# Kernel tuning notes

Hardware: AMD Instinct MI355X
Metric: run time of the kernel (lower is better)

The kernel has to match this reference:

```python
import jax, jax.numpy as jnp
import numpy as np

BS, L, H, HD, R, HID = 4, 2048, 12, 64, 16, 768


def setup_inputs() -> dict:
    key = jax.random.key(0)
    k0, k1, k2, k3 = jax.random.split(key, 4)
    xavier = np.sqrt(2.0 / (H + HD))  # xavier_normal_ on (H, HD)
    lin = 1.0 / np.sqrt(HID)
    return {
        "hidden_states": jax.random.normal(k0, (BS, L, HID), jnp.float32),
        "K1_w": jax.random.normal(k1, (HID, H * HD), jnp.float32) * lin,
        "K1_b": jnp.zeros((H * HD,), jnp.float32),
        "V1_w": jax.random.normal(k2, (HID, H * HD), jnp.float32) * lin,
        "V1_b": jnp.zeros((H * HD,), jnp.float32),
        "ReadingHead": jax.random.normal(k3, (H, HD), jnp.float32) * xavier,
        "bidirection_weight": jnp.full((1, 1, H, 1, 2 * R), 1.0 / (2 * R), jnp.float32),
    }


def _scan_mmap(valid_mask, reverse):
    # valid_mask: (bs, L, H) bool. Sequential register-shift scan over positions 1..L-1.
    bs, Ln, Hn = valid_mask.shape
    idxs = jnp.arange(1, Ln, dtype=jnp.int32)
    masks = jnp.swapaxes(valid_mask[:, 1:], 0, 1)  # (L-1, bs, H)
    if reverse:
        idxs = idxs[::-1]
        masks = masks[::-1]
    init = jnp.zeros((bs, R + 1, Hn), jnp.int32)

    def step(valids, xm):
        i, m = xm
        valids = valids.at[:, 0].set(i)  # slot 0 <- current index (matches in-place torch order)
        shifted = jnp.where(m[:, None, :], valids[:, :-1], valids[:, 1:])
        valids = valids.at[:, 1:].set(shifted)
        return valids, valids[:, 1:]

    _, out = jax.lax.scan(step, init, (idxs, masks))  # (L-1, bs, R, H)
    if reverse:
        out = out[::-1]
    out = jnp.concatenate([jnp.zeros((1, bs, R, Hn), jnp.int32), out], axis=0)
    return jnp.swapaxes(out, 0, 1)  # (bs, L, R, H)


def reference(hidden_states, K1_w, K1_b, V1_w, V1_b, ReadingHead, bidirection_weight):
    K1 = jax.nn.relu(hidden_states @ K1_w + K1_b).reshape(BS, L, H, HD)
    V1 = jax.nn.relu(hidden_states @ V1_w + V1_b).reshape(BS, L, H, HD)
    dot_products = jnp.einsum('blhn,hn->blh', K1, ReadingHead)
    valid_mask = dot_products > 0.5  # attn_var default branch
    fm = _scan_mmap(valid_mask, False).reshape(BS, L * R, H)
    bm = _scan_mmap(valid_mask, True).reshape(BS, L * R, H)
    V_forward = jnp.take_along_axis(V1, fm[..., None], axis=1).reshape(BS, L, R, H, HD)
    V_backward = jnp.take_along_axis(V1, bm[..., None], axis=1).reshape(BS, L, R, H, HD)
    w = bidirection_weight[0, 0, :, 0, :]  # (H, 2R); first R -> forward, last R -> backward
    ctx = (jnp.einsum('blrhd,hr->blhd', V_forward, w[:, :R])
           + jnp.einsum('blrhd,hr->blhd', V_backward, w[:, R:]))
    return ctx.reshape(BS, L, H * HD)
```

## Files before the change

### kernel.cpp

```cpp
#include <hip/hip_runtime.h>
#include <hip/hip_bf16.h>

#define BS 4
#define L 2048
#define H 12
#define HD 64
#define R 16
#define HID 768
#define MARGIN 0.02f
#define FIXCAP 16384
#define FIXGRID 1024

typedef __attribute__((ext_vector_type(8))) short s8v;
typedef __attribute__((ext_vector_type(4))) float f32x4;

static __device__ __forceinline__ unsigned short f2bf_bits(float f) {
    __hip_bfloat16 h = __float2bfloat16(f);
    return *reinterpret_cast<unsigned short*>(&h);
}

__global__ __launch_bounds__(256) void prep_kernel(
    const float* __restrict__ K1w, const float* __restrict__ V1w,
    __hip_bfloat16* __restrict__ WtK, __hip_bfloat16* __restrict__ WtV,
    int* __restrict__ fixcnt)
{
    if (blockIdx.x == 0 && threadIdx.x == 0) *fixcnt = 0;
    const int t = blockIdx.x;
    const int z = t / 576, rem = t % 576;
    const float* in = z ? V1w : K1w;
    __hip_bfloat16* out = z ? WtV : WtK;
    __shared__ float s[32][33];
    const int c = threadIdx.x & 31, r8 = threadIdx.x >> 5;
    const int kt = (rem / 24) * 32, nt = (rem % 24) * 32;
#pragma unroll
    for (int rr = 0; rr < 4; ++rr) {
        int k = r8 + rr * 8;
        s[k][c] = in[(size_t)(kt + k) * HID + nt + c];
    }
    __syncthreads();
#pragma unroll
    for (int rr = 0; rr < 4; ++rr) {
        int n = r8 + rr * 8;
        out[(size_t)(nt + n) * HID + kt + c] = __float2bfloat16(s[c][n]);
    }
}

__global__ __launch_bounds__(256) void gemm_fused(
    const float* __restrict__ A,
    const __hip_bfloat16* __restrict__ WtK,
    const __hip_bfloat16* __restrict__ WtV,
    const float* __restrict__ K1b,
    const float* __restrict__ V1b,
    const float* __restrict__ RH,
    float* __restrict__ dots,
    int* __restrict__ fixlist,
    int* __restrict__ fixcnt,
    __hip_bfloat16* __restrict__ C)
{
    __shared__ alignas(16) __hip_bfloat16 As[128 * 32];
    __shared__ alignas(16) __hip_bfloat16 Bs[128 * 32];

    const int tid = threadIdx.x;
    const bool isV = blockIdx.y < 6;
    const int m0 = blockIdx.x * 128;
    const int n0 = (isV ? blockIdx.y : blockIdx.y - 6) * 128;
    const __hip_bfloat16* Bt = isV ? WtV : WtK;

    const int wid = tid >> 6, lane = tid & 63;
    const int quad = lane >> 4, lm = lane & 15;
    const int wm = wid & 1, wn = wid >> 1;

    const int r0 = tid >> 2,        c0 = tid & 3;
    const int r1 = (tid + 256) >> 2, c1 = tid & 3;
    const int p0 = c0 ^ ((r0 >> 1) & 3);
    const int p1 = c1 ^ ((r1 >> 1) & 3);

    const float* gA0 = A + (size_t)(m0 + r0) * HID + c0 * 8;
    const float* gA1 = A + (size_t)(m0 + r1) * HID + c1 * 8;
    const __hip_bfloat16* gB0 = Bt + (size_t)(n0 + r0) * HID + c0 * 8;
    const __hip_bfloat16* gB1 = Bt + (size_t)(n0 + r1) * HID + c1 * 8;
    uint4* wA0 = (uint4*)&As[r0 * 32 + p0 * 8];
    uint4* wA1 = (uint4*)&As[r1 * 32 + p1 * 8];
    uint4* wB0 = (uint4*)&Bs[r0 * 32 + p0 * 8];
    uint4* wB1 = (uint4*)&Bs[r1 * 32 + p1 * 8];

    const int fsw = (lm >> 1) & 3;
    const __hip_bfloat16* pA = &As[(wm * 64 + lm) * 32 + ((quad ^ fsw) * 8)];
    const __hip_bfloat16* pB = &Bs[(wn * 64 + lm) * 32 + ((quad ^ fsw) * 8)];

    f32x4 acc[4][4] = {};

    float4 a00 = *(const float4*)gA0, a01 = *(const float4*)(gA0 + 4);
    float4 a10 = *(const float4*)gA1, a11 = *(const float4*)(gA1 + 4);
    uint4  b0  = *(const uint4*)gB0,  b1  = *(const uint4*)gB1;
    gA0 += 32; gA1 += 32; gB0 += 32; gB1 += 32;

    for (int it = 0; it < HID / 32; ++it) {
        union { unsigned short s[8]; uint4 v; } u0, u1;
        u0.s[0] = f2bf_bits(a00.x); u0.s[1] = f2bf_bits(a00.y);
        u0.s[2] = f2bf_bits(a00.z); u0.s[3] = f2bf_bits(a00.w);
        u0.s[4] = f2bf_bits(a01.x); u0.s[5] = f2bf_bits(a01.y);
        u0.s[6] = f2bf_bits(a01.z); u0.s[7] = f2bf_bits(a01.w);
        u1.s[0] = f2bf_bits(a10.x); u1.s[1] = f2bf_bits(a10.y);
        u1.s[2] = f2bf_bits(a10.z); u1.s[3] = f2bf_bits(a10.w);
        u1.s[4] = f2bf_bits(a11.x); u1.s[5] = f2bf_bits(a11.y);
        u1.s[6] = f2bf_bits(a11.z); u1.s[7] = f2bf_bits(a11.w);
        *wA0 = u0.v; *wA1 = u1.v;
        *wB0 = b0;   *wB1 = b1;
        __syncthreads();

        if (it + 1 < HID / 32) {
            a00 = *(const float4*)gA0; a01 = *(const float4*)(gA0 + 4);
            a10 = *(const float4*)gA1; a11 = *(const float4*)(gA1 + 4);
            b0  = *(const uint4*)gB0;  b1  = *(const uint4*)gB1;
            gA0 += 32; gA1 += 32; gB0 += 32; gB1 += 32;
        }

        s8v af[4], bf[4];
#pragma unroll
        for (int i = 0; i < 4; ++i) af[i] = *(const s8v*)(pA + i * 16 * 32);
#pragma unroll
        for (int j = 0; j < 4; ++j) bf[j] = *(const s8v*)(pB + j * 16 * 32);
#pragma unroll
        for (int i = 0; i < 4; ++i)
#pragma unroll
            for (int j = 0; j < 4; ++j)
                acc[i][j] = __builtin_amdgcn_mfma_f32_16x16x32_bf16(
                    af[i], bf[j], acc[i][j], 0, 0, 0);
        __syncthreads();
    }

    if (isV) {
#pragma unroll
        for (int i = 0; i < 4; ++i) {
            int row_b = m0 + wm * 64 + i * 16 + quad * 4;
#pragma unroll
            for (int j = 0; j < 4; ++j) {
                int col = n0 + wn * 64 + j * 16 + lm;
                float bsv = V1b[col];
#pragma unroll
                for (int reg = 0; reg < 4; ++reg) {
                    float v = acc[i][j][reg] + bsv;
                    C[(size_t)(row_b + reg) * HID + col] =
                        __float2bfloat16(fmaxf(v, 0.f));
                }
            }
        }
    } else {
        const int head = (n0 >> 6) + wn;
        float bj[4], rj[4];
#pragma unroll
        for (int j = 0; j < 4; ++j) {
            bj[j] = K1b[head * 64 + j * 16 + lm];
            rj[j] = RH[head * 64 + j * 16 + lm];
        }
#pragma unroll
        for (int i = 0; i < 4; ++i) {
            int row0 = m0 + wm * 64 + i * 16 + quad * 4;
#pragma unroll
            for (int reg = 0; reg < 4; ++reg) {
                float p = 0.f;
#pragma unroll
                for (int j = 0; j < 4; ++j)
                    p = fmaf(fmaxf(acc[i][j][reg] + bj[j], 0.f), rj[j], p);
                p += __shfl_xor(p, 1, 64);
                p += __shfl_xor(p, 2, 64);
                p += __shfl_xor(p, 4, 64);
                p += __shfl_xor(p, 8, 64);
                if (lm == 0) {
                    int row = row0 + reg;
                    int b = row >> 11, l = row & (L - 1);
                    dots[((b * H + head) << 11) + l] = p;
                    if (fabsf(p - 0.5f) < MARGIN) {
                        int idx = atomicAdd(fixcnt, 1);
                        if (idx < FIXCAP) fixlist[idx] = row * 16 + head;
                    }
                }
            }
        }
    }
}

__global__ __launch_bounds__(256) void fixup_kernel(
    const float* __restrict__ hs,
    const float* __restrict__ W,
    const float* __restrict__ bias,
    const float* __restrict__ RH,
    const int* __restrict__ fixlist,
    const int* __restrict__ fixcnt,
    float* __restrict__ dots)
{
    __shared__ float hrow[HID];
    __shared__ float psum[4][64];

    const int tid = threadIdx.x;
    const int n = min(*fixcnt, FIXCAP);

    for (int item = blockIdx.x; item < n; item += FIXGRID) {
        int packed = fixlist[item];
        int row = packed >> 4, head = packed & 15;
        int b = row >> 11, l = row & (L - 1);

#pragma unroll
        for (int i = 0; i < 3; ++i)
            hrow[tid + i * 256] = hs[(size_t)row * HID + tid + i * 256];
        __syncthreads();

        const int d = tid & 63, kq = tid >> 6;
        float a0 = 0.f, a1 = 0.f;
#pragma unroll 8
        for (int i = 0; i < 96; ++i) {
            int k = kq + i * 8;
            a0 = fmaf(W[(size_t)k * HID + head * 64 + d], hrow[k], a0);
            a1 = fmaf(W[(size_t)(k + 4) * HID + head * 64 + d], hrow[k + 4], a1);
        }
        psum[kq][d] = a0 + a1;
        __syncthreads();
        if (tid < 64) {
            float v = psum[0][tid] + psum[1][tid] + psum[2][tid] +
                      psum[3][tid] + bias[head * 64 + tid];
            v = fmaxf(v, 0.f) * RH[head * 64 + tid];
#pragma unroll
            for (int s = 1; s < 64; s <<= 1) v += __shfl_xor(v, s, 64);
            if (tid == 0) dots[((size_t)(b * H + head) << 11) + l] = v;
        }
        __syncthreads();
    }
}

__global__ __launch_bounds__(256) void scan_kernel(
    const float* __restrict__ dots,
    unsigned short* __restrict__ Pg,
    unsigned short* __restrict__ Sg)
{
    __shared__ int wsum[4];
    const int bh = blockIdx.x;
    const int tid = threadIdx.x;
    const int base = tid * 8;
    const int lane = tid & 63, w = tid >> 6;

    int m[8], c[8];
    int run = 0;
#pragma unroll
    for (int i = 0; i < 8; ++i) {
        int l = base + i;
        m[i] = (l >= 1 && dots[((size_t)bh << 11) + l] > 0.5f) ? 1 : 0;
        run += m[i];
        c[i] = run;
    }
    int sc = run;
#pragma unroll
    for (int s = 1; s < 64; s <<= 1) {
        int v = __shfl_up(sc, s, 64);
        if (lane >= s) sc += v;
    }
    if (lane == 63) wsum[w] = sc;
    __syncthreads();
    int woff = 0;
    for (int i = 0; i < 4; ++i) if (i < w) woff += wsum[i];
    const int ex = woff + sc - run;

    union { unsigned short s[8]; uint4 q; } up;
#pragma unroll
    for (int i = 0; i < 8; ++i) {
        int pc = ex + c[i];
        up.s[i] = (unsigned short)pc;
        if (m[i]) Sg[((size_t)bh << 11) + pc] = (unsigned short)(base + i);
    }
    *(uint4*)&Pg[((size_t)bh << 11) + base] = up.q;
}

__global__ __launch_bounds__(256) void gather_kernel(
    const __hip_bfloat16* __restrict__ V1,
    const unsigned short* __restrict__ Pg,
    const unsigned short* __restrict__ Sg,
    const float* __restrict__ bw,
    float* __restrict__ out)
{
    __shared__ __hip_bfloat16 Vs[97 * 72];
    __shared__ unsigned short Ptile[65];
    __shared__ short slots[64 * 32];
    __shared__ float sw[2 * R];
    __shared__ int sT;

    const int bh = blockIdx.y;
    const int b = bh / H, h = bh % H;
    const int l0 = blockIdx.x * 64;
    const int tid = threadIdx.x;

    if (tid < 65) {
        int l = l0 - 1 + tid;
        Ptile[tid] = (l >= 0) ? Pg[((size_t)bh << 11) + l] : (unsigned short)0;
    } else if (tid < 65 + 2 * R) {
        sw[tid - 65] = bw[h * (2 * R) + (tid - 65)];
    } else if (tid == 100) {
        sT = Pg[((size_t)bh << 11) + (L - 1)];
    }
    __syncthreads();

    const int T = sT;
    const int a = max(1, (int)Ptile[1] - (R - 1));
    const int bj = min(T, (int)Ptile[63] + R);
    const int nr = max(0, bj - a + 1);

    const __hip_bfloat16* Vbase = V1 + (size_t)b * L * HID + h * HD;
    for (int it = tid; it < (nr + 1) * 8; it += 256) {
        int slot = it >> 3, oct = it & 7;
        int row = slot ? (int)Sg[((size_t)bh << 11) + a + slot - 1] : 0;
        *(uint4*)&Vs[slot * 72 + oct * 8] =
            *(const uint4*)&Vbase[(size_t)row * HID + oct * 8];
    }
#pragma unroll
    for (int q = 0; q < 8; ++q) {
        int i = tid + q * 256;
        int ll = i >> 5, r = i & 31;
        int l = l0 + ll;
        int Pl = Ptile[1 + ll], Plm1 = Ptile[ll];
        int j, ok;
        if (r < R) { j = Pl - r;             ok = (l >= 1) && (j >= 1); }
        else       { j = Plm1 + 1 + (r - R); ok = (l >= 1) && (j <= T); }
        slots[i] = (short)(ok ? (j - a + 1) : 0);
    }
    __syncthreads();

    const int d8 = tid & 7, lg = tid >> 3;

#pragma unroll
    for (int li = 0; li < 2; ++li) {
        int ll = lg + 32 * li;
        int l = l0 + ll;
        float acc0 = 0.f, acc1 = 0.f, acc2 = 0.f, acc3 = 0.f;
        float acc4 = 0.f, acc5 = 0.f, acc6 = 0.f, acc7 = 0.f;
#pragma unroll
        for (int r = 0; r < 2 * R; ++r) {
            int slot = slots[ll * 32 + r];
            float wv = sw[r];
            uint4 uv = *(const uint4*)&Vs[slot * 72 + d8 * 8];
            acc0 = fmaf(wv, __uint_as_float(uv.x << 16), acc0);
            acc1 = fmaf(wv, __uint_as_float(uv.x & 0xffff0000u), acc1);
            acc2 = fmaf(wv, __uint_as_float(uv.y << 16), acc2);
            acc3 = fmaf(wv, __uint_as_float(uv.y & 0xffff0000u), acc3);
            acc4 = fmaf(wv, __uint_as_float(uv.z << 16), acc4);
            acc5 = fmaf(wv, __uint_as_float(uv.z & 0xffff0000u), acc5);
            acc6 = fmaf(wv, __uint_as_float(uv.w << 16), acc6);
            acc7 = fmaf(wv, __uint_as_float(uv.w & 0xffff0000u), acc7);
        }
        float* op = &out[((size_t)b * L + l) * HID + h * HD + d8 * 8];
        float4 o0, o1;
        o0.x = acc0; o0.y = acc1; o0.z = acc2; o0.w = acc3;
        o1.x = acc4; o1.y = acc5; o1.z = acc6; o1.w = acc7;
        *(float4*)op = o0;
        *(float4*)(op + 4) = o1;
    }
}

extern "C" void kernel_launch(void* const* d_in, const int* in_sizes, int n_in,
                              void* d_out, int out_size, void* d_ws, size_t ws_size,
                              hipStream_t stream) {
    const float* hs  = (const float*)d_in[0];
    const float* K1w = (const float*)d_in[1];
    const float* K1b = (const float*)d_in[2];
    const float* V1w = (const float*)d_in[3];
    const float* V1b = (const float*)d_in[4];
    const float* RH  = (const float*)d_in[5];
    const float* bw  = (const float*)d_in[6];
    float* out = (float*)d_out;

    char* ws = (char*)d_ws;
    __hip_bfloat16* WtV = (__hip_bfloat16*)ws;
    __hip_bfloat16* WtK = (__hip_bfloat16*)(ws + 1179648);
    __hip_bfloat16* V1  = (__hip_bfloat16*)(ws + 2359296);
    float* dots = (float*)(ws + 14942208);
    unsigned short* Pg = (unsigned short*)(ws + 15335424);
    unsigned short* Sg = (unsigned short*)(ws + 15532032);
    int* fixlist = (int*)(ws + 15728640);
    int* fixcnt  = (int*)(ws + 15794176);

    prep_kernel<<<2 * 24 * 24, 256, 0, stream>>>(K1w, V1w, WtK, WtV, fixcnt);
    gemm_fused<<<dim3(BS * L / 128, 12), 256, 0, stream>>>(
        hs, WtK, WtV, K1b, V1b, RH, dots, fixlist, fixcnt, V1);
    fixup_kernel<<<FIXGRID, 256, 0, stream>>>(hs, K1w, K1b, RH, fixlist, fixcnt, dots);
    scan_kernel<<<BS * H, 256, 0, stream>>>(dots, Pg, Sg);
    gather_kernel<<<dim3(L / 64, BS * H), 256, 0, stream>>>(V1, Pg, Sg, bw, out);
}
```

Baseline: 168.4 us.

## Share A tile across V and K projections in one 512-thread GEMM block

Restructures the fused GEMM so each 512-thread block computes the same 128 output columns for both the V and K projections from a shared 64-row A tile. Half the waves do V, half do K. This removes the duplicate fp32 load and bf16 conversion of hidden_states that happened when V and K were separate blocks. In exchange the M tile shrinks to 64, which lowers the MFMA-to-load ratio per wave, and only half the threads load A.

```diff
diff --git a/kernel.cpp b/kernel.cpp
--- a/kernel.cpp
+++ b/kernel.cpp
@@ -45,7 +45,7 @@
     }
 }
 
-__global__ __launch_bounds__(256) void gemm_fused(
+__global__ __launch_bounds__(512) void gemm_fused(
     const float* __restrict__ A,
     const __hip_bfloat16* __restrict__ WtK,
     const __hip_bfloat16* __restrict__ WtV,
@@ -57,72 +57,72 @@
     int* __restrict__ fixcnt,
     __hip_bfloat16* __restrict__ C)
 {
-    __shared__ alignas(16) __hip_bfloat16 As[128 * 32];
-    __shared__ alignas(16) __hip_bfloat16 Bs[128 * 32];
+    __shared__ alignas(16) __hip_bfloat16 As[64 * 32];
+    __shared__ alignas(16) __hip_bfloat16 BsV[128 * 32];
+    __shared__ alignas(16) __hip_bfloat16 BsK[128 * 32];
 
     const int tid = threadIdx.x;
-    const bool isV = blockIdx.y < 6;
-    const int m0 = blockIdx.x * 128;
-    const int n0 = (isV ? blockIdx.y : blockIdx.y - 6) * 128;
-    const __hip_bfloat16* Bt = isV ? WtV : WtK;
-
-    const int wid = tid >> 6, lane = tid & 63;
+    const int m0 = blockIdx.x * 64;
+    const int n0 = blockIdx.y * 128;
+
+    const int bmx = tid >> 8;
+    const int br = (tid & 255) >> 2, bc = tid & 3;
+    const int bp = bc ^ ((br >> 1) & 3);
+    const __hip_bfloat16* gB =
+        (bmx ? WtK : WtV) + (size_t)(n0 + br) * HID + bc * 8;
+    __hip_bfloat16* BsD = bmx ? BsK : BsV;
+    uint4* wB0 = (uint4*)(BsD + br * 32 + bp * 8);
+    uint4* wB1 = (uint4*)(BsD + (br + 64) * 32 + bp * 8);
+
+    const int ar = tid >> 2, ac = tid & 3;
+    const int ap = ac ^ ((ar >> 1) & 3);
+    const float* gA = A + (size_t)(m0 + (ar & 63)) * HID + ac * 8;
+    uint4* wA = (uint4*)(As + (ar & 63) * 32 + ap * 8);
+
+    const int w = tid >> 6, lane = tid & 63;
+    const bool isV = w < 4;
+    const int wl = w & 3, wm2 = wl & 1, wn2 = wl >> 1;
     const int quad = lane >> 4, lm = lane & 15;
-    const int wm = wid & 1, wn = wid >> 1;
-
-    const int r0 = tid >> 2,        c0 = tid & 3;
-    const int r1 = (tid + 256) >> 2, c1 = tid & 3;
-    const int p0 = c0 ^ ((r0 >> 1) & 3);
-    const int p1 = c1 ^ ((r1 >> 1) & 3);
-
-    const float* gA0 = A + (size_t)(m0 + r0) * HID + c0 * 8;
-    const float* gA1 = A + (size_t)(m0 + r1) * HID + c1 * 8;
-    const __hip_bfloat16* gB0 = Bt + (size_t)(n0 + r0) * HID + c0 * 8;
-    const __hip_bfloat16* gB1 = Bt + (size_t)(n0 + r1) * HID + c1 * 8;
-    uint4* wA0 = (uint4*)&As[r0 * 32 + p0 * 8];
-    uint4* wA1 = (uint4*)&As[r1 * 32 + p1 * 8];
-    uint4* wB0 = (uint4*)&Bs[r0 * 32 + p0 * 8];
-    uint4* wB1 = (uint4*)&Bs[r1 * 32 + p1 * 8];
-
     const int fsw = (lm >> 1) & 3;
-    const __hip_bfloat16* pA = &As[(wm * 64 + lm) * 32 + ((quad ^ fsw) * 8)];
-    const __hip_bfloat16* pB = &Bs[(wn * 64 + lm) * 32 + ((quad ^ fsw) * 8)];
-
-    f32x4 acc[4][4] = {};
-
-    float4 a00 = *(const float4*)gA0, a01 = *(const float4*)(gA0 + 4);
-    float4 a10 = *(const float4*)gA1, a11 = *(const float4*)(gA1 + 4);
-    uint4  b0  = *(const uint4*)gB0,  b1  = *(const uint4*)gB1;
-    gA0 += 32; gA1 += 32; gB0 += 32; gB1 += 32;
+    const __hip_bfloat16* pA = &As[(wm2 * 32 + lm) * 32 + ((quad ^ fsw) * 8)];
+    const __hip_bfloat16* pB =
+        (isV ? BsV : BsK) + (wn2 * 64 + lm) * 32 + ((quad ^ fsw) * 8);
+
+    f32x4 acc[2][4] = {};
+
+    float4 a0, a1;
+    uint4 bv0 = *(const uint4*)gB;
+    uint4 bv1 = *(const uint4*)(gB + (size_t)64 * HID);
+    if (tid < 256) { a0 = *(const float4*)gA; a1 = *(const float4*)(gA + 4); }
+    gA += 32; gB += 32;
 
     for (int it = 0; it < HID / 32; ++it) {
-        union { unsigned short s[8]; uint4 v; } u0, u1;
-        u0.s[0] = f2bf_bits(a00.x); u0.s[1] = f2bf_bits(a00.y);
-        u0.s[2] = f2bf_bits(a00.z); u0.s[3] = f2bf_bits(a00.w);
-        u0.s[4] = f2bf_bits(a01.x); u0.s[5] = f2bf_bits(a01.y);
-        u0.s[6] = f2bf_bits(a01.z); u0.s[7] = f2bf_bits(a01.w);
-        u1.s[0] = f2bf_bits(a10.x); u1.s[1] = f2bf_bits(a10.y);
-        u1.s[2] = f2bf_bits(a10.z); u1.s[3] = f2bf_bits(a10.w);
-        u1.s[4] = f2bf_bits(a11.x); u1.s[5] = f2bf_bits(a11.y);
-        u1.s[6] = f2bf_bits(a11.z); u1.s[7] = f2bf_bits(a11.w);
-        *wA0 = u0.v; *wA1 = u1.v;
-        *wB0 = b0;   *wB1 = b1;
+        if (tid < 256) {
+            union { unsigned short s[8]; uint4 v; } u;
+            u.s[0] = f2bf_bits(a0.x); u.s[1] = f2bf_bits(a0.y);
+            u.s[2] = f2bf_bits(a0.z); u.s[3] = f2bf_bits(a0.w);
+            u.s[4] = f2bf_bits(a1.x); u.s[5] = f2bf_bits(a1.y);
+            u.s[6] = f2bf_bits(a1.z); u.s[7] = f2bf_bits(a1.w);
+            *wA = u.v;
+        }
+        *wB0 = bv0;
+        *wB1 = bv1;
         __syncthreads();
 
         if (it + 1 < HID / 32) {
-            a00 = *(const float4*)gA0; a01 = *(const float4*)(gA0 + 4);
-            a10 = *(const float4*)gA1; a11 = *(const float4*)(gA1 + 4);
-            b0  = *(const uint4*)gB0;  b1  = *(const uint4*)gB1;
-            gA0 += 32; gA1 += 32; gB0 += 32; gB1 += 32;
-        }
-
-        s8v af[4], bf[4];
-#pragma unroll
-        for (int i = 0; i < 4; ++i) af[i] = *(const s8v*)(pA + i * 16 * 32);
+            bv0 = *(const uint4*)gB;
+            bv1 = *(const uint4*)(gB + (size_t)64 * HID);
+            if (tid < 256) { a0 = *(const float4*)gA; a1 = *(const float4*)(gA + 4); }
+            gA += 32; gB += 32;
+        }
+
+        s8v af[2], bf[4];
+#pragma unroll
+        for (int i = 0; i < 2; ++i) af[i] = *(const s8v*)(pA + i * 16 * 32);
 #pragma unroll
         for (int j = 0; j < 4; ++j) bf[j] = *(const s8v*)(pB + j * 16 * 32);
 #pragma unroll
-        for (int i = 0; i < 4; ++i)
+        for (int i = 0; i < 2; ++i)
 #pragma unroll
             for (int j = 0; j < 4; ++j)
                 acc[i][j] = __builtin_amdgcn_mfma_f32_16x16x32_bf16(
@@ -132,11 +132,11 @@
 
     if (isV) {
 #pragma unroll
-        for (int i = 0; i < 4; ++i) {
-            int row_b = m0 + wm * 64 + i * 16 + quad * 4;
+        for (int i = 0; i < 2; ++i) {
+            int row_b = m0 + wm2 * 32 + i * 16 + quad * 4;
 #pragma unroll
             for (int j = 0; j < 4; ++j) {
-                int col = n0 + wn * 64 + j * 16 + lm;
+                int col = n0 + wn2 * 64 + j * 16 + lm;
                 float bsv = V1b[col];
 #pragma unroll
                 for (int reg = 0; reg < 4; ++reg) {
@@ -147,7 +147,7 @@
             }
         }
     } else {
-        const int head = (n0 >> 6) + wn;
+        const int head = 2 * blockIdx.y + wn2;
         float bj[4], rj[4];
 #pragma unroll
         for (int j = 0; j < 4; ++j) {
@@ -155,8 +155,8 @@
             rj[j] = RH[head * 64 + j * 16 + lm];
         }
 #pragma unroll
-        for (int i = 0; i < 4; ++i) {
-            int row0 = m0 + wm * 64 + i * 16 + quad * 4;
+        for (int i = 0; i < 2; ++i) {
+            int row0 = m0 + wm2 * 32 + i * 16 + quad * 4;
 #pragma unroll
             for (int reg = 0; reg < 4; ++reg) {
                 float p = 0.f;
@@ -377,7 +377,7 @@
     int* fixcnt  = (int*)(ws + 15794176);
 
     prep_kernel<<<2 * 24 * 24, 256, 0, stream>>>(K1w, V1w, WtK, WtV, fixcnt);
-    gemm_fused<<<dim3(BS * L / 128, 12), 256, 0, stream>>>(
+    gemm_fused<<<dim3(BS * L / 64, 6), 512, 0, stream>>>(
         hs, WtK, WtV, K1b, V1b, RH, dots, fixlist, fixcnt, V1);
     fixup_kernel<<<FIXGRID, 256, 0, stream>>>(hs, K1w, K1b, RH, fixlist, fixcnt, dots);
     scan_kernel<<<BS * H, 256, 0, stream>>>(dots, Pg, Sg);
```

Measured after the change: 174.9 us. +3.9%, slower.

## Pre-convert activations to bf16 and stage GEMM tiles via direct global-to-LDS loads

Applied to the files above, without the earlier changes.

The prep kernel now also converts hidden_states to bf16 into scratch space borrowed from the output buffer. The GEMM then loads both A and B tiles with global_load_lds, writing straight into LDS with a swizzled column layout, instead of going through registers with per-element fp32-to-bf16 conversion. This removes conversion ALU work and register staging from the GEMM main loop and halves A-tile read bytes. The cost is an extra pass over the activations, and the loop loses its register prefetch of the next K-tile, so loads are no longer overlapped with MFMA work.

```diff
diff --git a/kernel.cpp b/kernel.cpp
--- a/kernel.cpp
+++ b/kernel.cpp
@@ -14,6 +14,11 @@
 typedef __attribute__((ext_vector_type(8))) short s8v;
 typedef __attribute__((ext_vector_type(4))) float f32x4;
 
+typedef __attribute__((address_space(1))) const void as1_void;
+typedef __attribute__((address_space(3))) void as3_void;
+#define GLOAD_LDS16(g, l) \
+    __builtin_amdgcn_global_load_lds((as1_void*)(g), (as3_void*)(l), 16, 0, 0)
+
 static __device__ __forceinline__ unsigned short f2bf_bits(float f) {
     __hip_bfloat16 h = __float2bfloat16(f);
     return *reinterpret_cast<unsigned short*>(&h);
@@ -21,32 +26,44 @@
 
 __global__ __launch_bounds__(256) void prep_kernel(
     const float* __restrict__ K1w, const float* __restrict__ V1w,
+    const float* __restrict__ hs,
     __hip_bfloat16* __restrict__ WtK, __hip_bfloat16* __restrict__ WtV,
+    __hip_bfloat16* __restrict__ Abf,
     int* __restrict__ fixcnt)
 {
-    if (blockIdx.x == 0 && threadIdx.x == 0) *fixcnt = 0;
-    const int t = blockIdx.x;
-    const int z = t / 576, rem = t % 576;
-    const float* in = z ? V1w : K1w;
-    __hip_bfloat16* out = z ? WtV : WtK;
-    __shared__ float s[32][33];
-    const int c = threadIdx.x & 31, r8 = threadIdx.x >> 5;
-    const int kt = (rem / 24) * 32, nt = (rem % 24) * 32;
-#pragma unroll
-    for (int rr = 0; rr < 4; ++rr) {
-        int k = r8 + rr * 8;
-        s[k][c] = in[(size_t)(kt + k) * HID + nt + c];
-    }
-    __syncthreads();
-#pragma unroll
-    for (int rr = 0; rr < 4; ++rr) {
-        int n = r8 + rr * 8;
-        out[(size_t)(nt + n) * HID + kt + c] = __float2bfloat16(s[c][n]);
+    const int blk = blockIdx.x;
+    if (blk == 0 && threadIdx.x == 0) *fixcnt = 0;
+
+    if (blk < 1152) {
+        const int z = blk / 576, rem = blk % 576;
+        const float* in = z ? V1w : K1w;
+        __hip_bfloat16* out = z ? WtV : WtK;
+        __shared__ float s[32][33];
+        const int c = threadIdx.x & 31, r8 = threadIdx.x >> 5;
+        const int kt = (rem / 24) * 32, nt = (rem % 24) * 32;
+#pragma unroll
+        for (int rr = 0; rr < 4; ++rr) {
+            int k = r8 + rr * 8;
+            s[k][c] = in[(size_t)(kt + k) * HID + nt + c];
+        }
+        __syncthreads();
+#pragma unroll
+        for (int rr = 0; rr < 4; ++rr) {
+            int n = r8 + rr * 8;
+            out[(size_t)(nt + n) * HID + kt + c] = __float2bfloat16(s[c][n]);
+        }
+    } else {
+        int i = ((blk - 1152) * 256 + threadIdx.x) * 4;
+        float4 v = *(const float4*)&hs[i];
+        ushort4 o;
+        o.x = f2bf_bits(v.x); o.y = f2bf_bits(v.y);
+        o.z = f2bf_bits(v.z); o.w = f2bf_bits(v.w);
+        *(ushort4*)&Abf[i] = o;
     }
 }
 
 __global__ __launch_bounds__(256) void gemm_fused(
-    const float* __restrict__ A,
+    const __hip_bfloat16* __restrict__ A,
     const __hip_bfloat16* __restrict__ WtK,
     const __hip_bfloat16* __restrict__ WtV,
     const float* __restrict__ K1b,
@@ -70,19 +87,18 @@
     const int quad = lane >> 4, lm = lane & 15;
     const int wm = wid & 1, wn = wid >> 1;
 
-    const int r0 = tid >> 2,        c0 = tid & 3;
-    const int r1 = (tid + 256) >> 2, c1 = tid & 3;
-    const int p0 = c0 ^ ((r0 >> 1) & 3);
-    const int p1 = c1 ^ ((r1 >> 1) & 3);
-
-    const float* gA0 = A + (size_t)(m0 + r0) * HID + c0 * 8;
-    const float* gA1 = A + (size_t)(m0 + r1) * HID + c1 * 8;
-    const __hip_bfloat16* gB0 = Bt + (size_t)(n0 + r0) * HID + c0 * 8;
-    const __hip_bfloat16* gB1 = Bt + (size_t)(n0 + r1) * HID + c1 * 8;
-    uint4* wA0 = (uint4*)&As[r0 * 32 + p0 * 8];
-    uint4* wA1 = (uint4*)&As[r1 * 32 + p1 * 8];
-    uint4* wB0 = (uint4*)&Bs[r0 * 32 + p0 * 8];
-    uint4* wB1 = (uint4*)&Bs[r1 * 32 + p1 * 8];
+    const int rsub = lane >> 2;
+    const int csw  = (lane & 3) ^ ((lane >> 3) & 3);
+    const __hip_bfloat16* gA0 =
+        A + (size_t)(m0 + 32 * wid + rsub) * HID + csw * 8;
+    const __hip_bfloat16* gA1 = gA0 + (size_t)16 * HID;
+    const __hip_bfloat16* gB0 =
+        Bt + (size_t)(n0 + 32 * wid + rsub) * HID + csw * 8;
+    const __hip_bfloat16* gB1 = gB0 + (size_t)16 * HID;
+    __hip_bfloat16* lA0 = &As[(32 * wid) * 32];
+    __hip_bfloat16* lA1 = &As[(32 * wid + 16) * 32];
+    __hip_bfloat16* lB0 = &Bs[(32 * wid) * 32];
+    __hip_bfloat16* lB1 = &Bs[(32 * wid + 16) * 32];
 
     const int fsw = (lm >> 1) & 3;
     const __hip_bfloat16* pA = &As[(wm * 64 + lm) * 32 + ((quad ^ fsw) * 8)];
@@ -90,37 +106,21 @@
 
     f32x4 acc[4][4] = {};
 
-    float4 a00 = *(const float4*)gA0, a01 = *(const float4*)(gA0 + 4);
-    float4 a10 = *(const float4*)gA1, a11 = *(const float4*)(gA1 + 4);
-    uint4  b0  = *(const uint4*)gB0,  b1  = *(const uint4*)gB1;
-    gA0 += 32; gA1 += 32; gB0 += 32; gB1 += 32;
-
-    for (int it = 0; it < HID / 32; ++it) {
-        union { unsigned short s[8]; uint4 v; } u0, u1;
-        u0.s[0] = f2bf_bits(a00.x); u0.s[1] = f2bf_bits(a00.y);
-        u0.s[2] = f2bf_bits(a00.z); u0.s[3] = f2bf_bits(a00.w);
-        u0.s[4] = f2bf_bits(a01.x); u0.s[5] = f2bf_bits(a01.y);
-        u0.s[6] = f2bf_bits(a01.z); u0.s[7] = f2bf_bits(a01.w);
-        u1.s[0] = f2bf_bits(a10.x); u1.s[1] = f2bf_bits(a10.y);
-        u1.s[2] = f2bf_bits(a10.z); u1.s[3] = f2bf_bits(a10.w);
-        u1.s[4] = f2bf_bits(a11.x); u1.s[5] = f2bf_bits(a11.y);
-        u1.s[6] = f2bf_bits(a11.z); u1.s[7] = f2bf_bits(a11.w);
-        *wA0 = u0.v; *wA1 = u1.v;
-        *wB0 = b0;   *wB1 = b1;
-        __syncthreads();
-
-        if (it + 1 < HID / 32) {
-            a00 = *(const float4*)gA0; a01 = *(const float4*)(gA0 + 4);
-            a10 = *(const float4*)gA1; a11 = *(const float4*)(gA1 + 4);
-            b0  = *(const uint4*)gB0;  b1  = *(const uint4*)gB1;
-            gA0 += 32; gA1 += 32; gB0 += 32; gB1 += 32;
-        }
+    for (int k0 = 0; k0 < HID; k0 += 32) {
+        GLOAD_LDS16(gA0, lA0);
+        GLOAD_LDS16(gA1, lA1);
+        GLOAD_LDS16(gB0, lB0);
+        GLOAD_LDS16(gB1, lB1);
+        gA0 += 32; gA1 += 32; gB0 += 32; gB1 += 32;
+        __syncthreads();
 
         s8v af[4], bf[4];
 #pragma unroll
-        for (int i = 0; i < 4; ++i) af[i] = *(const s8v*)(pA + i * 16 * 32);
-#pragma unroll
-        for (int j = 0; j < 4; ++j) bf[j] = *(const s8v*)(pB + j * 16 * 32);
+        for (int i = 0; i < 4; ++i)
+            af[i] = *(const s8v*)(pA + i * 16 * 32);
+#pragma unroll
+        for (int j = 0; j < 4; ++j)
+            bf[j] = *(const s8v*)(pB + j * 16 * 32);
 #pragma unroll
         for (int i = 0; i < 4; ++i)
 #pragma unroll
@@ -366,6 +366,8 @@
     const float* bw  = (const float*)d_in[6];
     float* out = (float*)d_out;
 
+    __hip_bfloat16* Abf = (__hip_bfloat16*)d_out;
+
     char* ws = (char*)d_ws;
     __hip_bfloat16* WtV = (__hip_bfloat16*)ws;
     __hip_bfloat16* WtK = (__hip_bfloat16*)(ws + 1179648);
@@ -376,9 +378,10 @@
     int* fixlist = (int*)(ws + 15728640);
     int* fixcnt  = (int*)(ws + 15794176);
 
-    prep_kernel<<<2 * 24 * 24, 256, 0, stream>>>(K1w, V1w, WtK, WtV, fixcnt);
+    prep_kernel<<<1152 + (BS * L * HID) / (256 * 4), 256, 0, stream>>>(
+        K1w, V1w, hs, WtK, WtV, Abf, fixcnt);
     gemm_fused<<<dim3(BS * L / 128, 12), 256, 0, stream>>>(
-        hs, WtK, WtV, K1b, V1b, RH, dots, fixlist, fixcnt, V1);
+        Abf, WtK, WtV, K1b, V1b, RH, dots, fixlist, fixcnt, V1);
     fixup_kernel<<<FIXGRID, 256, 0, stream>>>(hs, K1w, K1b, RH, fixlist, fixcnt, dots);
     scan_kernel<<<BS * H, 256, 0, stream>>>(dots, Pg, Sg);
     gather_kernel<<<dim3(L / 64, BS * H), 256, 0, stream>>>(V1, Pg, Sg, bw, out);
```

Measured after the change: 170.4 us. No clear change (+1.2%).
